# Kernel optimization log

Measured on AMD Instinct MI355X. Metric: run time of the kernel, lower is better.

The kernel has to match this reference:

```python
import jax, jax.numpy as jnp
import numpy as np

N_NODES = 3000
N_FEAT = 2
N_UNITS = 64
BATCH = 16
K_DIFF = 2  # max_diffusion_step


def _supports(adj):
    # dual_random_walk: (D^-1 A)^T and (D'^-1 A^T)^T, rows with zero degree -> 0
    def rw_T(A):
        d = A.sum(axis=1)
        d_inv = jnp.where(d > 0, 1.0 / d, 0.0)
        return (d_inv[:, None] * A).T  # (N, N)
    return [rw_T(adj), rw_T(adj.T)]


def _gconv(inputs, state, supports, W, b, num_nodes):
    # inputs: (B, N*F), state: (B, N*U)
    B = inputs.shape[0]
    x = jnp.concatenate([inputs.reshape(B, num_nodes, -1),
                         state.reshape(B, num_nodes, -1)], axis=2)  # (B, N, C)
    x0 = x.transpose(1, 2, 0)  # (N, C, B)
    mats = [x0]
    for S in supports:
        x1 = jnp.einsum('mn,ncb->mcb', S, x0)
        mats.append(x1)
        xk_1, xk_2 = x1, x0
        for _ in range(2, K_DIFF + 1):
            x2 = 2.0 * jnp.einsum('mn,ncb->mcb', S, xk_1) - xk_2  # Chebyshev recurrence
            mats.append(x2)
            xk_1, xk_2 = x2, xk_1
    xs = jnp.stack(mats, axis=0)  # (M, N, C, B)
    M, _, C, _ = xs.shape
    xs = xs.transpose(3, 1, 2, 0).reshape(B * num_nodes, C * M)
    out = xs @ W + b  # (B*N, O)
    return out.reshape(B, num_nodes * W.shape[1])


def setup_inputs() -> dict:
    key = jax.random.key(0)
    k1, k2, k3, k4, k5 = jax.random.split(key, 5)
    C = N_FEAT + N_UNITS          # 66
    M = 2 * K_DIFF + 1            # 5 (two supports)
    xw = lambda k, s: jax.random.normal(k, s, dtype=jnp.float32) * jnp.sqrt(2.0 / (s[0] + s[1]))
    return {
        "inputs": jax.random.normal(k1, (BATCH, N_NODES * N_FEAT), dtype=jnp.float32),
        "hx": jax.random.normal(k2, (BATCH, N_NODES * N_UNITS), dtype=jnp.float32),
        "adj_mx": jax.random.uniform(k3, (N_NODES, N_NODES), dtype=jnp.float32),
        "W_gate": xw(k4, (C * M, 2 * N_UNITS)),
        "b_gate": jnp.ones((2 * N_UNITS,), dtype=jnp.float32),  # bias_start=1.0
        "W_cand": xw(k5, (C * M, N_UNITS)),
        "b_cand": jnp.zeros((N_UNITS,), dtype=jnp.float32),
        "num_nodes": N_NODES,
    }


def reference(inputs, hx, adj_mx, W_gate, b_gate, W_cand, b_cand, num_nodes):
    supports = _supports(adj_mx)
    B = inputs.shape[0]
    value = jax.nn.sigmoid(_gconv(inputs, hx, supports, W_gate, b_gate, num_nodes))
    value = value.reshape(B, num_nodes, 2 * N_UNITS)
    r, u = value[..., :N_UNITS], value[..., N_UNITS:]
    r = r.reshape(B, num_nodes * N_UNITS)
    u = u.reshape(B, num_nodes * N_UNITS)
    c = jnp.tanh(_gconv(inputs, r * hx, supports, W_cand, b_cand, num_nodes))
    new_state = u * hx + (1.0 - u) * c
    return new_state
```

## Files before the change

kernel.cpp:

```cpp
#include <hip/hip_runtime.h>
#include <cstdint>
#include <cstddef>


typedef unsigned short u16;
typedef __bf16 bf16x8 __attribute__((ext_vector_type(8)));
typedef u16 u16x8 __attribute__((ext_vector_type(8)));
typedef u16 u16x4 __attribute__((ext_vector_type(4)));
typedef float f32x4 __attribute__((ext_vector_type(4)));

#define NND 3000
#define KP  3008
#define NBX 16
#define NCBP 1152
#define KW  330
#define KWP 352

__device__ __forceinline__ float b2f(u16 x) { return (float)__builtin_bit_cast(__bf16, x); }
__device__ __forceinline__ u16 f2b(float f) { return __builtin_bit_cast(u16, (__bf16)f); }

__device__ __forceinline__ int getmode(const u16* bgp) { return (bgp[0] == 0x3F80) ? 0 : 1; }

__device__ __forceinline__ float rdf(const void* p, size_t i, int mode) {
  return mode ? ((const float*)p)[i] : b2f(((const u16*)p)[i]);
}

__device__ __forceinline__ void gll16(const u16* g, void* l) {
  __builtin_amdgcn_global_load_lds(
      (const __attribute__((address_space(1))) unsigned int*)g,
      (__attribute__((address_space(3))) unsigned int*)l, 16, 0, 0);
}

__device__ __forceinline__ void ld4(const void* A, int rg, int cg, int mode,
                                    float& v0, float& v1, float& v2, float& v3) {
  v0 = v1 = v2 = v3 = 0.f;
  if (rg >= NND) return;
  if (cg + 3 < NND) {
    if (mode) {
      f32x4 f = *(const f32x4*)((const float*)A + (size_t)rg * NND + cg);
      v0 = f[0]; v1 = f[1]; v2 = f[2]; v3 = f[3];
    } else {
      u16x4 u = *(const u16x4*)((const u16*)A + (size_t)rg * NND + cg);
      v0 = b2f(u[0]); v1 = b2f(u[1]); v2 = b2f(u[2]); v3 = b2f(u[3]);
    }
  } else {
    if (cg + 0 < NND) v0 = rdf(A, (size_t)rg * NND + cg + 0, mode);
    if (cg + 1 < NND) v1 = rdf(A, (size_t)rg * NND + cg + 1, mode);
    if (cg + 2 < NND) v2 = rdf(A, (size_t)rg * NND + cg + 2, mode);
    if (cg + 3 < NND) v3 = rdf(A, (size_t)rg * NND + cg + 3, mode);
  }
}

struct PrepParams {
  const void* A;
  const void* Wg; const void* Wc;
  const void* inp; const void* hx;
  const u16* bgp;
  float* d0sum; float* d1sum;
  u16* Wtg; u16* Wtc;
  u16* xtg; u16* xtc; u16* chx;
};

__global__ __launch_bounds__(256) void k_prep(PrepParams p) {
  const int bid = blockIdx.x, t = threadIdx.x;
  const int mode = getmode(p.bgp);

  if (bid < 2209) {
    __shared__ float ldsx[64 * 65];
    const int R = (bid / 47) * 64, C = (bid % 47) * 64;
#pragma unroll
    for (int ph = 0; ph < 4; ++ph) {
      int idx = t + ph * 256;
      int r = idx >> 4, c4 = (idx & 15) * 4;
      float v0, v1, v2, v3;
      ld4(p.A, R + r, C + c4, mode, v0, v1, v2, v3);
      ldsx[r * 65 + c4 + 0] = v0;
      ldsx[r * 65 + c4 + 1] = v1;
      ldsx[r * 65 + c4 + 2] = v2;
      ldsx[r * 65 + c4 + 3] = v3;
    }
    __syncthreads();
    if (t < 64) {
      int rg = R + t;
      if (rg < NND) {
        float s = 0.f;
#pragma unroll 8
        for (int c = 0; c < 64; ++c) s += ldsx[t * 65 + c];
        atomicAdd(&p.d0sum[rg], s);
      }
    } else if (t < 128) {
      int cg = C + (t - 64);
      if (cg < NND) {
        float s = 0.f;
#pragma unroll 8
        for (int r = 0; r < 64; ++r) s += ldsx[r * 65 + (t - 64)];
        atomicAdd(&p.d1sum[cg], s);
      }
    }
    return;
  }
  if (bid < 2473) {
    const int idx = (bid - 2209) * 256 + t;
    if (idx < 128 * KWP) {
      int o = idx / KWP, k = idx - o * KWP;
      float v = (k < KW) ? rdf(p.Wg, (size_t)k * 128 + o, mode) : 0.f;
      p.Wtg[idx] = f2b(v);
    } else if (idx < 192 * KWP) {
      int i2 = idx - 128 * KWP;
      int o = i2 / KWP, k = i2 - o * KWP;
      float v = (k < KW) ? rdf(p.Wc, (size_t)k * 64 + o, mode) : 0.f;
      p.Wtc[i2] = f2b(v);
    }
    return;
  }
  {
    const int idx = bid - 2473;
    const int nt = idx % 24, b = idx / 24;
    const int n0 = nt * 128;
    __shared__ __align__(16) u16 hxl[128 * 72];
#pragma unroll
    for (int i = 0; i < 4; ++i) {
      int id = t + 256 * i;
      int nl = id >> 3, og = (id & 7) * 8;
      int ng = n0 + nl; if (ng > NND - 1) ng = NND - 1;
      const size_t base = (size_t)b * 192000 + (size_t)ng * 64 + og;
      u16x8 v;
      if (mode) {
        const float* h = (const float*)p.hx + base;
        f32x4 lo = *(const f32x4*)h, hi = *(const f32x4*)(h + 4);
        v[0] = f2b(lo[0]); v[1] = f2b(lo[1]); v[2] = f2b(lo[2]); v[3] = f2b(lo[3]);
        v[4] = f2b(hi[0]); v[5] = f2b(hi[1]); v[6] = f2b(hi[2]); v[7] = f2b(hi[3]);
      } else {
        v = *(const u16x8*)&((const u16*)p.hx)[base];
      }
      *(u16x8*)&hxl[nl * 72 + og] = v;
    }
    __syncthreads();
#pragma unroll
    for (int i = 0; i < 4; ++i) {
      int id = t + 256 * i;
      int nl = id >> 3, og = (id & 7) * 8;
      int ng = n0 + nl;
      if (ng < NND)
        *(u16x8*)&p.chx[(size_t)b * 192000 + (size_t)ng * 64 + og] = *(u16x8*)&hxl[nl * 72 + og];
    }
#pragma unroll
    for (int i = 0; i < 4; ++i) {
      int id = t + 256 * i;
      int u = id >> 4, ngrp = (id & 15) * 8;
      int nb = n0 + ngrp;
      if (nb < KP) {
        u16x8 v;
#pragma unroll
        for (int e = 0; e < 8; ++e) {
          int ng = nb + e;
          v[e] = (ng < NND) ? hxl[(ngrp + e) * 72 + u] : (u16)0;
        }
        *(u16x8*)&p.xtg[(size_t)((2 + u) * 16 + b) * KP + nb] = v;
      }
    }
    if (t < 32) {
      int c = t >> 4, ngrp = (t & 15) * 8;
      int nb = n0 + ngrp;
      if (nb < KP) {
        u16x8 v;
#pragma unroll
        for (int e = 0; e < 8; ++e) {
          int ng = nb + e;
          v[e] = (ng < NND) ? f2b(rdf(p.inp, (size_t)b * 6000 + (size_t)ng * 2 + c, mode)) : (u16)0;
        }
        *(u16x8*)&p.xtg[(size_t)(c * 16 + b) * KP + nb] = v;
        *(u16x8*)&p.xtc[(size_t)(c * 16 + b) * KP + nb] = v;
      }
    }
    if (nt == 23 && t < 64) {
      u16x8 z = {0, 0, 0, 0, 0, 0, 0, 0};
      *(u16x8*)&p.xtc[(size_t)((2 + t) * 16 + b) * KP + NND] = z;
    }
  }
}

__global__ __launch_bounds__(256) void k_sboth(const void* __restrict__ A, const float* __restrict__ d0sum,
                                               const float* __restrict__ d1sum,
                                               u16* __restrict__ S0, u16* __restrict__ S1,
                                               const u16* __restrict__ bgp) {
  __shared__ float ldsx[64 * 65];
  __shared__ float inv1c[64];
  __shared__ float inv0r[64];
  const int C = blockIdx.x * 64, R = blockIdx.y * 64, t = threadIdx.x;
  const int mode = getmode(bgp);
  if (t < 64) {
    int cg = C + t;
    float ds = (cg < NND) ? d1sum[cg] : 0.f;
    inv1c[t] = ds > 0.f ? 1.f / ds : 0.f;
  } else if (t < 128) {
    int rg = R + (t - 64);
    float ds = (rg < NND) ? d0sum[rg] : 0.f;
    inv0r[t - 64] = ds > 0.f ? 1.f / ds : 0.f;
  }
#pragma unroll
  for (int ph = 0; ph < 4; ++ph) {
    int idx = t + ph * 256;
    int r = idx >> 4, c4 = (idx & 15) * 4;
    float v0, v1, v2, v3;
    ld4(A, R + r, C + c4, mode, v0, v1, v2, v3);
    ldsx[r * 65 + c4 + 0] = v0;
    ldsx[r * 65 + c4 + 1] = v1;
    ldsx[r * 65 + c4 + 2] = v2;
    ldsx[r * 65 + c4 + 3] = v3;
  }
  __syncthreads();
#pragma unroll
  for (int ph = 0; ph < 4; ++ph) {
    int idx = t + ph * 256;
    int mr = idx >> 4, nc4 = (idx & 15) * 4;
    int m1 = R + mr;
    if (m1 < NND) {
      u16x4 v;
#pragma unroll
      for (int i = 0; i < 4; ++i) v[i] = f2b(ldsx[mr * 65 + nc4 + i] * inv1c[nc4 + i]);
      *(u16x4*)&S1[(size_t)m1 * KP + C + nc4] = v;
    }
    int m0_ = C + mr;
    if (m0_ < NND) {
      u16x4 v;
#pragma unroll
      for (int i = 0; i < 4; ++i) v[i] = f2b(ldsx[(nc4 + i) * 65 + mr] * inv0r[nc4 + i]);
      *(u16x4*)&S0[(size_t)m0_ * KP + R + nc4] = v;
    }
  }
}

struct GemmAParams {
  const u16* A0; const u16* A1;
  const u16* B0; const u16* B1;
  u16* D0; u16* D1;
  const u16* X;
  int mode;
};

__global__ __launch_bounds__(256, 2) void k_gemmA(GemmAParams p) {
  __shared__ __align__(16) u16 lds[32768];
  const int bid = blockIdx.x;
  const int x8 = bid & 7, g = bid >> 3;
  const int slot = g / 9, n_idx = g - slot * 9;
  const int strip = x8 * 6 + slot;
  const int m_idx = strip >> 1, z = strip & 1;
  const u16* Sp = z ? p.A1 : p.A0;
  const u16* Bp = z ? p.B1 : p.B0;
  u16* Dp = z ? p.D1 : p.D0;
  const int n0 = n_idx * 128;
  const int m0 = m_idx * 128;
  const int t = threadIdx.x;
  const int lane = t & 63, w = t >> 6;
  const int wr = w >> 1, wc = w & 1;
  const int l15 = lane & 15, lq = lane >> 4;
  const int x7 = l15 & 7;

  const u16* gsrc[8];
  int lbase[8];
#pragma unroll
  for (int q = 0; q < 8; ++q) {
    const int c = t + 256 * q;
    if (c < 1024) {
      const int row = c >> 3, grp = c & 7;
      int mg = m0 + row; if (mg > NND - 1) mg = NND - 1;
      gsrc[q] = Sp + (size_t)mg * KP + ((grp ^ (row & 7)) << 3);
      lbase[q] = q * 4096 + w * 1024;
    } else {
      const int c2 = c - 1024;
      const int row = c2 >> 3, grp = c2 & 7;
      gsrc[q] = Bp + (size_t)(n0 + row) * KP + ((grp ^ (row & 7)) << 3);
      lbase[q] = 16384 + (q - 4) * 4096 + w * 1024;
    }
  }

  f32x4 acc[4][4];
#pragma unroll
  for (int i = 0; i < 4; ++i)
#pragma unroll
    for (int j = 0; j < 4; ++j) acc[i][j] = (f32x4){0.f, 0.f, 0.f, 0.f};

  auto STAGE = [&](int buf) {
    char* L = (char*)lds + buf * 32768;
#pragma unroll
    for (int q = 0; q < 8; ++q) { gll16(gsrc[q], (void*)(L + lbase[q])); gsrc[q] += 64; }
  };
  auto STEP = [&](int buf) {
    const u16* L = lds + buf * 16384;
    bf16x8 af[4][2], bf[4][2];
#pragma unroll
    for (int kk = 0; kk < 2; ++kk) {
#pragma unroll
      for (int i = 0; i < 4; ++i)
        af[i][kk] = *(const bf16x8*)&L[(wr * 64 + i * 16 + l15) * 64 + (((kk * 4 + lq) ^ x7) << 3)];
#pragma unroll
      for (int j = 0; j < 4; ++j)
        bf[j][kk] = *(const bf16x8*)&L[8192 + (wc * 64 + j * 16 + l15) * 64 + (((kk * 4 + lq) ^ x7) << 3)];
    }
#pragma unroll
    for (int kk = 0; kk < 2; ++kk)
#pragma unroll
      for (int i = 0; i < 4; ++i)
#pragma unroll
        for (int j = 0; j < 4; ++j)
          acc[i][j] = __builtin_amdgcn_mfma_f32_16x16x32_bf16(af[i][kk], bf[j][kk], acc[i][j], 0, 0, 0);
  };

  STAGE(0);
  for (int ks = 0; ks < 47; ++ks) {
    const int buf = ks & 1;
    if (ks < 46) {
      STAGE(buf ^ 1);
      asm volatile("s_waitcnt vmcnt(8)" ::: "memory");
    } else {
      asm volatile("s_waitcnt vmcnt(0)" ::: "memory");
    }
    __builtin_amdgcn_s_barrier();
    __builtin_amdgcn_sched_barrier(0);
    STEP(buf);
    __builtin_amdgcn_sched_barrier(0);
    __builtin_amdgcn_s_barrier();
  }

  __syncthreads();
  u16* Tw = &lds[w * 4608];
#pragma unroll
  for (int i = 0; i < 4; ++i)
#pragma unroll
    for (int j = 0; j < 4; ++j)
#pragma unroll
      for (int r = 0; r < 4; ++r) {
        int miw = i * 16 + lq * 4 + r;
        int niw = j * 16 + l15;
        float v = acc[i][j][r];
        if (m0 + wr * 64 + miw >= NND) v = 0.f;
        Tw[niw * 72 + miw] = f2b(v);
      }
  const int row8 = lane >> 3, colg = (lane & 7) * 8;
#pragma unroll
  for (int ph = 0; ph < 8; ++ph) {
    int nrow = ph * 8 + row8;
    int n_g = n0 + wc * 64 + nrow;
    int m_b = m0 + wr * 64 + colg;
    if (m_b < KP) {
      u16x8 y = *(u16x8*)&Tw[nrow * 72 + colg];
      if (p.mode) {
        const u16x8 x = *(const u16x8*)&p.X[(size_t)n_g * KP + m_b];
#pragma unroll
        for (int e = 0; e < 8; ++e) y[e] = f2b(2.f * b2f(y[e]) - b2f(x[e]));
      }
      *(u16x8*)&Dp[(size_t)n_g * KP + m_b] = y;
    }
  }
}

struct GateParams {
  const u16* xall;
  const u16* Wt;
  const void* bias;
  const u16* hx;
  u16* xtc;
  u16* ut;
  const u16* bgp;
};

__global__ __launch_bounds__(256, 2) void k_gate(GateParams p) {
  __shared__ __align__(16) u16 Al[128 * 40];
  __shared__ __align__(16) u16 Bl[64 * 40];
  __shared__ __align__(16) u16 hxl[64 * 72];
  __shared__ int rowA[KWP];
  const int b = blockIdx.y, n0 = blockIdx.x * 64;
  const int t = threadIdx.x, lane = t & 63, w = t >> 6, wr = w >> 1, wc = w & 1;
  const int l15 = lane & 15, lq = lane >> 4;
  const int mode = getmode(p.bgp);

  for (int k = t; k < KWP; k += 256) {
    int c = k / 5, mt = k - c * 5;
    rowA[k] = (k < KW) ? (mt * NCBP + c * 16 + b) * KP : 0;
  }
#pragma unroll
  for (int i = 0; i < 2; ++i) {
    int id = t + 256 * i;
    int nl = id >> 3, og = (id & 7) * 8;
    int ng = n0 + nl; if (ng > NND - 1) ng = NND - 1;
    *(u16x8*)&hxl[nl * 72 + og] = *(const u16x8*)&p.hx[(size_t)b * 192000 + (size_t)ng * 64 + og];
  }
  __syncthreads();

  f32x4 acc[4][2];
#pragma unroll
  for (int i = 0; i < 4; ++i)
#pragma unroll
    for (int j = 0; j < 2; ++j) acc[i][j] = (f32x4){0.f, 0.f, 0.f, 0.f};

  u16x8 aReg[2]; u16x8 bReg;
#pragma unroll
  for (int hh = 0; hh < 2; ++hh) {
    int id = t + 256 * hh;
    int r = id >> 2, g = id & 3;
    aReg[hh] = *(const u16x8*)&p.Wt[(size_t)r * KWP + g * 8];
  }
#pragma unroll
  for (int e = 0; e < 8; ++e) {
    int k = w * 8 + e;
    u16 x = p.xall[(size_t)rowA[k] + n0 + lane];
    bReg[e] = (k < KW) ? x : (u16)0;
  }

  for (int ks = 0; ks < 11; ++ks) {
    __syncthreads();
#pragma unroll
    for (int hh = 0; hh < 2; ++hh) {
      int id = t + 256 * hh;
      int r = id >> 2, g = id & 3;
      *(u16x8*)&Al[r * 40 + g * 8] = aReg[hh];
    }
    *(u16x8*)&Bl[lane * 40 + w * 8] = bReg;
    __syncthreads();

    if (ks + 1 < 11) {
      const int k0 = (ks + 1) * 32;
#pragma unroll
      for (int hh = 0; hh < 2; ++hh) {
        int id = t + 256 * hh;
        int r = id >> 2, g = id & 3;
        aReg[hh] = *(const u16x8*)&p.Wt[(size_t)r * KWP + k0 + g * 8];
      }
#pragma unroll
      for (int e = 0; e < 8; ++e) {
        int k = k0 + w * 8 + e;
        u16 x = p.xall[(size_t)rowA[k] + n0 + lane];
        bReg[e] = (k < KW) ? x : (u16)0;
      }
    }

    bf16x8 af[4], bf[2];
#pragma unroll
    for (int i = 0; i < 4; ++i) af[i] = *(const bf16x8*)&Al[(wr * 64 + i * 16 + l15) * 40 + lq * 8];
#pragma unroll
    for (int j = 0; j < 2; ++j) bf[j] = *(const bf16x8*)&Bl[(wc * 32 + j * 16 + l15) * 40 + lq * 8];
#pragma unroll
    for (int i = 0; i < 4; ++i)
#pragma unroll
      for (int j = 0; j < 2; ++j)
        acc[i][j] = __builtin_amdgcn_mfma_f32_16x16x32_bf16(af[i], bf[j], acc[i][j], 0, 0, 0);
  }

#pragma unroll
  for (int i = 0; i < 4; ++i)
#pragma unroll
    for (int j = 0; j < 2; ++j)
#pragma unroll
      for (int r = 0; r < 4; ++r) {
        int o = wr * 64 + i * 16 + lq * 4 + r;
        int nl = wc * 32 + j * 16 + l15;
        int ng = n0 + nl;
        if (ng < NND) {
          float v = acc[i][j][r] + rdf(p.bias, o, mode);
          float s = 1.f / (1.f + __expf(-v));
          if (o < 64) {
            float rh = s * b2f(hxl[nl * 72 + o]);
            p.xtc[(size_t)((o + 2) * 16 + b) * KP + ng] = f2b(rh);
          } else {
            p.ut[(size_t)b * 192000 + (size_t)(o - 64) * NND + ng] = f2b(s);
          }
        }
      }
}

struct CandParams {
  const u16* xall;
  const u16* Wt;
  const void* bias;
  const u16* hx;
  const u16* ut;
  void* out;
  const u16* bgp;
};

__global__ __launch_bounds__(256, 2) void k_cand(CandParams p) {
  __shared__ __align__(16) u16 Al[64 * 40];
  __shared__ __align__(16) u16 Bl[64 * 40];
  __shared__ __align__(16) u16 hxl[64 * 72];
  __shared__ __align__(16) u16 newl[64 * 72];
  __shared__ int rowA[KWP];
  const int b = blockIdx.y, n0 = blockIdx.x * 64;
  const int t = threadIdx.x, lane = t & 63, w = t >> 6, wr = w >> 1, wc = w & 1;
  const int l15 = lane & 15, lq = lane >> 4;
  const int mode = getmode(p.bgp);

  for (int k = t; k < KWP; k += 256) {
    int c = k / 5, mt = k - c * 5;
    rowA[k] = (k < KW) ? (mt * NCBP + c * 16 + b) * KP : 0;
  }
#pragma unroll
  for (int i = 0; i < 2; ++i) {
    int id = t + 256 * i;
    int nl = id >> 3, og = (id & 7) * 8;
    int ng = n0 + nl; if (ng > NND - 1) ng = NND - 1;
    *(u16x8*)&hxl[nl * 72 + og] = *(const u16x8*)&p.hx[(size_t)b * 192000 + (size_t)ng * 64 + og];
  }
  __syncthreads();

  f32x4 acc[2][2];
#pragma unroll
  for (int i = 0; i < 2; ++i)
#pragma unroll
    for (int j = 0; j < 2; ++j) acc[i][j] = (f32x4){0.f, 0.f, 0.f, 0.f};

  u16x8 aReg; u16x8 bReg;
  {
    int r = t >> 2, g = t & 3;
    aReg = *(const u16x8*)&p.Wt[(size_t)r * KWP + g * 8];
  }
#pragma unroll
  for (int e = 0; e < 8; ++e) {
    int k = w * 8 + e;
    u16 x = p.xall[(size_t)rowA[k] + n0 + lane];
    bReg[e] = (k < KW) ? x : (u16)0;
  }

  for (int ks = 0; ks < 11; ++ks) {
    __syncthreads();
    {
      int r = t >> 2, g = t & 3;
      *(u16x8*)&Al[r * 40 + g * 8] = aReg;
    }
    *(u16x8*)&Bl[lane * 40 + w * 8] = bReg;
    __syncthreads();

    if (ks + 1 < 11) {
      const int k0 = (ks + 1) * 32;
      {
        int r = t >> 2, g = t & 3;
        aReg = *(const u16x8*)&p.Wt[(size_t)r * KWP + k0 + g * 8];
      }
#pragma unroll
      for (int e = 0; e < 8; ++e) {
        int k = k0 + w * 8 + e;
        u16 x = p.xall[(size_t)rowA[k] + n0 + lane];
        bReg[e] = (k < KW) ? x : (u16)0;
      }
    }

    bf16x8 af[2], bf[2];
#pragma unroll
    for (int i = 0; i < 2; ++i) af[i] = *(const bf16x8*)&Al[(wr * 32 + i * 16 + l15) * 40 + lq * 8];
#pragma unroll
    for (int j = 0; j < 2; ++j) bf[j] = *(const bf16x8*)&Bl[(wc * 32 + j * 16 + l15) * 40 + lq * 8];
#pragma unroll
    for (int i = 0; i < 2; ++i)
#pragma unroll
      for (int j = 0; j < 2; ++j)
        acc[i][j] = __builtin_amdgcn_mfma_f32_16x16x32_bf16(af[i], bf[j], acc[i][j], 0, 0, 0);
  }

#pragma unroll
  for (int i = 0; i < 2; ++i)
#pragma unroll
    for (int j = 0; j < 2; ++j)
#pragma unroll
      for (int r = 0; r < 4; ++r) {
        int o = wr * 32 + i * 16 + lq * 4 + r;
        int nl = wc * 32 + j * 16 + l15;
        int ng = n0 + nl; int ngc = ng > NND - 1 ? NND - 1 : ng;
        float v = acc[i][j][r] + rdf(p.bias, o, mode);
        float c = tanhf(v);
        float u = b2f(p.ut[(size_t)b * 192000 + (size_t)o * NND + ngc]);
        float h = b2f(hxl[nl * 72 + o]);
        newl[nl * 72 + o] = f2b(u * h + (1.f - u) * c);
      }
  __syncthreads();
#pragma unroll
  for (int i = 0; i < 2; ++i) {
    int id = t + 256 * i;
    int nl = id >> 3, og = (id & 7) * 8;
    int ng = n0 + nl;
    if (ng < NND) {
      u16x8 v = *(u16x8*)&newl[nl * 72 + og];
      if (mode) {
        float* of = (float*)p.out + (size_t)b * 192000 + (size_t)ng * 64 + og;
        f32x4 lo = {b2f(v[0]), b2f(v[1]), b2f(v[2]), b2f(v[3])};
        f32x4 hi = {b2f(v[4]), b2f(v[5]), b2f(v[6]), b2f(v[7])};
        *(f32x4*)of = lo;
        *(f32x4*)(of + 4) = hi;
      } else {
        *(u16x8*)&((u16*)p.out)[(size_t)b * 192000 + (size_t)ng * 64 + og] = v;
      }
    }
  }
}


extern "C" void kernel_launch(void* const* d_in, const int* in_sizes, int n_in,
                              void* d_out, int out_size, void* d_ws, size_t ws_size,
                              hipStream_t stream) {
  const size_t SLP = (size_t)NCBP * KP;
  size_t off = 0;
  auto alloc = [&](size_t bytes) {
    void* pp = (char*)d_ws + off;
    off += (bytes + 255) & ~(size_t)255;
    return pp;
  };
  u16* S0  = (u16*)alloc((size_t)NND * KP * 2);
  u16* S1  = (u16*)alloc((size_t)NND * KP * 2);
  u16* Xg  = (u16*)alloc(5 * SLP * 2);
  u16* Xc  = (u16*)alloc(5 * SLP * 2);
  u16* Ut  = (u16*)alloc((size_t)NBX * 64 * NND * 2);
  u16* Wtg = (u16*)alloc((size_t)128 * KWP * 2);
  u16* Wtc = (u16*)alloc((size_t)64 * KWP * 2);
  float* dsums = (float*)alloc(2 * NND * 4);
  u16* cHx  = (u16*)alloc((size_t)3072000 * 2);
  (void)in_sizes; (void)n_in; (void)out_size;

  if (ws_size < off) return;

  float* d0sum = dsums;
  float* d1sum = dsums + NND;

  u16* Xtg = Xg;            u16* Y1 = Xg + SLP;  u16* Z2 = Xg + 2 * SLP;
  u16* Y3 = Xg + 3 * SLP;   u16* Z4 = Xg + 4 * SLP;
  u16* Xtc = Xc;            u16* Y1c = Xc + SLP; u16* Z2c = Xc + 2 * SLP;
  u16* Y3c = Xc + 3 * SLP;  u16* Z4c = Xc + 4 * SLP;

  const void* inp = d_in[0];
  const void* hx  = d_in[1];
  const void* adj = d_in[2];
  const void* Wg  = d_in[3];
  const u16*  bg  = (const u16*)d_in[4];
  const void* Wc  = d_in[5];
  const void* bc  = d_in[6];

  hipMemsetAsync(dsums, 0, 2 * NND * 4, stream);
  PrepParams pp = {adj, Wg, Wc, inp, hx, bg, d0sum, d1sum, Wtg, Wtc, Xtg, Xtc, cHx};
  k_prep<<<2857, 256, 0, stream>>>(pp);
  k_sboth<<<dim3(47, 47), 256, 0, stream>>>(adj, d0sum, d1sum, S0, S1, bg);

  GemmAParams g1 = {S0, S1, Xtg, Xtg, Y1, Y3, nullptr, 0};
  k_gemmA<<<432, 256, 0, stream>>>(g1);
  GemmAParams g2 = {S0, S1, Y1, Y3, Z2, Z4, Xtg, 1};
  k_gemmA<<<432, 256, 0, stream>>>(g2);

  GateParams gp = {Xg, Wtg, bg, cHx, Xtc, Ut, bg};
  k_gate<<<dim3(47, NBX), 256, 0, stream>>>(gp);

  GemmAParams g3 = {S0, S1, Xtc, Xtc, Y1c, Y3c, nullptr, 0};
  k_gemmA<<<432, 256, 0, stream>>>(g3);
  GemmAParams g4 = {S0, S1, Y1c, Y3c, Z2c, Z4c, Xtc, 1};
  k_gemmA<<<432, 256, 0, stream>>>(g4);

  CandParams cp = {Xc, Wtc, bc, cHx, Ut, d_out, bg};
  k_cand<<<dim3(47, NBX), 256, 0, stream>>>(cp);
}
```

Baseline: 350.6 us.

## Fuse pipeline into one cooperative persistent kernel with grid syncs

Replaces the memset plus seven separate kernel launches with a single cooperative persistent kernel of 432 blocks. Stages are separated by grid.sync and each block loops over that stage's jobs. The degree sums are now computed directly instead of with atomics: a row reduction per warp and a strided column reduction. This removes launch gaps and the memset, but it caps parallelism at 432 blocks for the prep and S-build stages, and the column-sum walks memory in a strided pattern.

```diff
diff --git a/kernel.cpp b/kernel.cpp
--- a/kernel.cpp
+++ b/kernel.cpp
@@ -1,6 +1,9 @@
 #include <hip/hip_runtime.h>
+#include <hip/hip_cooperative_groups.h>
 #include <cstdint>
 #include <cstddef>
+
+namespace cg = cooperative_groups;
 
 
 typedef unsigned short u16;
@@ -15,6 +18,7 @@
 #define NCBP 1152
 #define KW  330
 #define KWP 352
+#define NBLK 432
 
 __device__ __forceinline__ float b2f(u16 x) { return (float)__builtin_bit_cast(__bf16, x); }
 __device__ __forceinline__ u16 f2b(float f) { return __builtin_bit_cast(u16, (__bf16)f); }
@@ -51,151 +55,156 @@
   }
 }
 
-struct PrepParams {
+struct MegaParams {
   const void* A;
   const void* Wg; const void* Wc;
   const void* inp; const void* hx;
   const u16* bgp;
+  const void* bcb;
   float* d0sum; float* d1sum;
   u16* Wtg; u16* Wtc;
-  u16* xtg; u16* xtc; u16* chx;
+  u16* Xg; u16* Xc;
+  u16* chx; u16* Ut;
+  u16* S0; u16* S1;
+  void* out;
 };
 
-__global__ __launch_bounds__(256) void k_prep(PrepParams p) {
-  const int bid = blockIdx.x, t = threadIdx.x;
-  const int mode = getmode(p.bgp);
-
-  if (bid < 2209) {
-    __shared__ float ldsx[64 * 65];
-    const int R = (bid / 47) * 64, C = (bid % 47) * 64;
-#pragma unroll
-    for (int ph = 0; ph < 4; ++ph) {
-      int idx = t + ph * 256;
-      int r = idx >> 4, c4 = (idx & 15) * 4;
-      float v0, v1, v2, v3;
-      ld4(p.A, R + r, C + c4, mode, v0, v1, v2, v3);
-      ldsx[r * 65 + c4 + 0] = v0;
-      ldsx[r * 65 + c4 + 1] = v1;
-      ldsx[r * 65 + c4 + 2] = v2;
-      ldsx[r * 65 + c4 + 3] = v3;
-    }
-    __syncthreads();
-    if (t < 64) {
-      int rg = R + t;
-      if (rg < NND) {
-        float s = 0.f;
-#pragma unroll 8
-        for (int c = 0; c < 64; ++c) s += ldsx[t * 65 + c];
-        atomicAdd(&p.d0sum[rg], s);
-      }
-    } else if (t < 128) {
-      int cg = C + (t - 64);
-      if (cg < NND) {
-        float s = 0.f;
-#pragma unroll 8
-        for (int r = 0; r < 64; ++r) s += ldsx[r * 65 + (t - 64)];
-        atomicAdd(&p.d1sum[cg], s);
-      }
-    }
-    return;
-  }
-  if (bid < 2473) {
-    const int idx = (bid - 2209) * 256 + t;
-    if (idx < 128 * KWP) {
-      int o = idx / KWP, k = idx - o * KWP;
-      float v = (k < KW) ? rdf(p.Wg, (size_t)k * 128 + o, mode) : 0.f;
-      p.Wtg[idx] = f2b(v);
-    } else if (idx < 192 * KWP) {
-      int i2 = idx - 128 * KWP;
-      int o = i2 / KWP, k = i2 - o * KWP;
-      float v = (k < KW) ? rdf(p.Wc, (size_t)k * 64 + o, mode) : 0.f;
-      p.Wtc[i2] = f2b(v);
-    }
-    return;
-  }
-  {
-    const int idx = bid - 2473;
-    const int nt = idx % 24, b = idx / 24;
-    const int n0 = nt * 128;
-    __shared__ __align__(16) u16 hxl[128 * 72];
-#pragma unroll
-    for (int i = 0; i < 4; ++i) {
-      int id = t + 256 * i;
-      int nl = id >> 3, og = (id & 7) * 8;
-      int ng = n0 + nl; if (ng > NND - 1) ng = NND - 1;
-      const size_t base = (size_t)b * 192000 + (size_t)ng * 64 + og;
+__device__ void prep_rowsum(int job, int t, int mode, const MegaParams& p) {
+  const int row = job * 4 + (t >> 6);
+  const int lane = t & 63;
+  float s = 0.f;
+  if (mode) {
+    const float* a = (const float*)p.A + (size_t)row * NND;
+    for (int i = lane; i < 750; i += 64) {
+      f32x4 v = *(const f32x4*)(a + 4 * i);
+      s += v[0] + v[1] + v[2] + v[3];
+    }
+  } else {
+    const u16* a = (const u16*)p.A + (size_t)row * NND;
+    for (int i = lane; i < 750; i += 64) {
+      u16x4 v = *(const u16x4*)(a + 4 * i);
+      s += b2f(v[0]) + b2f(v[1]) + b2f(v[2]) + b2f(v[3]);
+    }
+  }
+  for (int off = 32; off; off >>= 1) s += __shfl_down(s, off, 64);
+  if (lane == 0) p.d0sum[row] = s;
+}
+
+__device__ void prep_colsum(int job, int t, int mode, const MegaParams& p, u16* smem) {
+  float* red = (float*)smem;
+  const int c0 = job * 64;
+  const int lane = t & 63, g = t >> 6;
+  const int col = c0 + lane;
+  float s = 0.f;
+  if (col < NND) {
+    if (mode) {
+      const float* a = (const float*)p.A;
+      for (int rg = g; rg < NND; rg += 4) s += a[(size_t)rg * NND + col];
+    } else {
+      const u16* a = (const u16*)p.A;
+      for (int rg = g; rg < NND; rg += 4) s += b2f(a[(size_t)rg * NND + col]);
+    }
+  }
+  __syncthreads();
+  red[t] = s;
+  __syncthreads();
+  if (t < 64 && c0 + t < NND)
+    p.d1sum[c0 + t] = red[t] + red[t + 64] + red[t + 128] + red[t + 192];
+}
+
+__device__ void prep_wt2(int job, int t, int mode, const MegaParams& p) {
+  const int idx = job * 256 + t;
+  if (idx < 128 * KWP) {
+    int o = idx / KWP, k = idx - o * KWP;
+    float v = (k < KW) ? rdf(p.Wg, (size_t)k * 128 + o, mode) : 0.f;
+    p.Wtg[idx] = f2b(v);
+  } else if (idx < 192 * KWP) {
+    int i2 = idx - 128 * KWP;
+    int o = i2 / KWP, k = i2 - o * KWP;
+    float v = (k < KW) ? rdf(p.Wc, (size_t)k * 64 + o, mode) : 0.f;
+    p.Wtc[i2] = f2b(v);
+  }
+}
+
+__device__ void prep_buildx(int job, int t, int mode, const MegaParams& p, u16* smem) {
+  u16* hxl = smem;
+  const int nt = job % 24, b = job / 24;
+  const int n0 = nt * 128;
+  __syncthreads();
+#pragma unroll
+  for (int i = 0; i < 4; ++i) {
+    int id = t + 256 * i;
+    int nl = id >> 3, og = (id & 7) * 8;
+    int ng = n0 + nl; if (ng > NND - 1) ng = NND - 1;
+    const size_t base = (size_t)b * 192000 + (size_t)ng * 64 + og;
+    u16x8 v;
+    if (mode) {
+      const float* h = (const float*)p.hx + base;
+      f32x4 lo = *(const f32x4*)h, hi = *(const f32x4*)(h + 4);
+      v[0] = f2b(lo[0]); v[1] = f2b(lo[1]); v[2] = f2b(lo[2]); v[3] = f2b(lo[3]);
+      v[4] = f2b(hi[0]); v[5] = f2b(hi[1]); v[6] = f2b(hi[2]); v[7] = f2b(hi[3]);
+    } else {
+      v = *(const u16x8*)&((const u16*)p.hx)[base];
+    }
+    *(u16x8*)&hxl[nl * 72 + og] = v;
+  }
+  __syncthreads();
+#pragma unroll
+  for (int i = 0; i < 4; ++i) {
+    int id = t + 256 * i;
+    int nl = id >> 3, og = (id & 7) * 8;
+    int ng = n0 + nl;
+    if (ng < NND)
+      *(u16x8*)&p.chx[(size_t)b * 192000 + (size_t)ng * 64 + og] = *(u16x8*)&hxl[nl * 72 + og];
+  }
+#pragma unroll
+  for (int i = 0; i < 4; ++i) {
+    int id = t + 256 * i;
+    int u = id >> 4, ngrp = (id & 15) * 8;
+    int nb = n0 + ngrp;
+    if (nb < KP) {
       u16x8 v;
-      if (mode) {
-        const float* h = (const float*)p.hx + base;
-        f32x4 lo = *(const f32x4*)h, hi = *(const f32x4*)(h + 4);
-        v[0] = f2b(lo[0]); v[1] = f2b(lo[1]); v[2] = f2b(lo[2]); v[3] = f2b(lo[3]);
-        v[4] = f2b(hi[0]); v[5] = f2b(hi[1]); v[6] = f2b(hi[2]); v[7] = f2b(hi[3]);
-      } else {
-        v = *(const u16x8*)&((const u16*)p.hx)[base];
-      }
-      *(u16x8*)&hxl[nl * 72 + og] = v;
-    }
-    __syncthreads();
-#pragma unroll
-    for (int i = 0; i < 4; ++i) {
-      int id = t + 256 * i;
-      int nl = id >> 3, og = (id & 7) * 8;
-      int ng = n0 + nl;
-      if (ng < NND)
-        *(u16x8*)&p.chx[(size_t)b * 192000 + (size_t)ng * 64 + og] = *(u16x8*)&hxl[nl * 72 + og];
-    }
-#pragma unroll
-    for (int i = 0; i < 4; ++i) {
-      int id = t + 256 * i;
-      int u = id >> 4, ngrp = (id & 15) * 8;
-      int nb = n0 + ngrp;
-      if (nb < KP) {
-        u16x8 v;
-#pragma unroll
-        for (int e = 0; e < 8; ++e) {
-          int ng = nb + e;
-          v[e] = (ng < NND) ? hxl[(ngrp + e) * 72 + u] : (u16)0;
-        }
-        *(u16x8*)&p.xtg[(size_t)((2 + u) * 16 + b) * KP + nb] = v;
-      }
-    }
-    if (t < 32) {
-      int c = t >> 4, ngrp = (t & 15) * 8;
-      int nb = n0 + ngrp;
-      if (nb < KP) {
-        u16x8 v;
-#pragma unroll
-        for (int e = 0; e < 8; ++e) {
-          int ng = nb + e;
-          v[e] = (ng < NND) ? f2b(rdf(p.inp, (size_t)b * 6000 + (size_t)ng * 2 + c, mode)) : (u16)0;
-        }
-        *(u16x8*)&p.xtg[(size_t)(c * 16 + b) * KP + nb] = v;
-        *(u16x8*)&p.xtc[(size_t)(c * 16 + b) * KP + nb] = v;
-      }
-    }
-    if (nt == 23 && t < 64) {
-      u16x8 z = {0, 0, 0, 0, 0, 0, 0, 0};
-      *(u16x8*)&p.xtc[(size_t)((2 + t) * 16 + b) * KP + NND] = z;
-    }
-  }
-}
-
-__global__ __launch_bounds__(256) void k_sboth(const void* __restrict__ A, const float* __restrict__ d0sum,
-                                               const float* __restrict__ d1sum,
-                                               u16* __restrict__ S0, u16* __restrict__ S1,
-                                               const u16* __restrict__ bgp) {
-  __shared__ float ldsx[64 * 65];
-  __shared__ float inv1c[64];
-  __shared__ float inv0r[64];
-  const int C = blockIdx.x * 64, R = blockIdx.y * 64, t = threadIdx.x;
-  const int mode = getmode(bgp);
+#pragma unroll
+      for (int e = 0; e < 8; ++e) {
+        int ng = nb + e;
+        v[e] = (ng < NND) ? hxl[(ngrp + e) * 72 + u] : (u16)0;
+      }
+      *(u16x8*)&p.Xg[(size_t)((2 + u) * 16 + b) * KP + nb] = v;
+    }
+  }
+  if (t < 32) {
+    int c = t >> 4, ngrp = (t & 15) * 8;
+    int nb = n0 + ngrp;
+    if (nb < KP) {
+      u16x8 v;
+#pragma unroll
+      for (int e = 0; e < 8; ++e) {
+        int ng = nb + e;
+        v[e] = (ng < NND) ? f2b(rdf(p.inp, (size_t)b * 6000 + (size_t)ng * 2 + c, mode)) : (u16)0;
+      }
+      *(u16x8*)&p.Xg[(size_t)(c * 16 + b) * KP + nb] = v;
+      *(u16x8*)&p.Xc[(size_t)(c * 16 + b) * KP + nb] = v;
+    }
+  }
+  if (nt == 23 && t < 64) {
+    u16x8 z = {0, 0, 0, 0, 0, 0, 0, 0};
+    *(u16x8*)&p.Xc[(size_t)((2 + t) * 16 + b) * KP + NND] = z;
+  }
+}
+
+__device__ void sboth_job(int job, int t, int mode, const MegaParams& p, u16* smem) {
+  float* ldsx = (float*)smem;
+  float* inv1c = ldsx + 64 * 65;
+  float* inv0r = inv1c + 64;
+  const int C = (job % 47) * 64, R = (job / 47) * 64;
+  __syncthreads();
   if (t < 64) {
     int cg = C + t;
-    float ds = (cg < NND) ? d1sum[cg] : 0.f;
+    float ds = (cg < NND) ? p.d1sum[cg] : 0.f;
     inv1c[t] = ds > 0.f ? 1.f / ds : 0.f;
   } else if (t < 128) {
     int rg = R + (t - 64);
-    float ds = (rg < NND) ? d0sum[rg] : 0.f;
+    float ds = (rg < NND) ? p.d0sum[rg] : 0.f;
     inv0r[t - 64] = ds > 0.f ? 1.f / ds : 0.f;
   }
 #pragma unroll
@@ -203,7 +212,7 @@
     int idx = t + ph * 256;
     int r = idx >> 4, c4 = (idx & 15) * 4;
     float v0, v1, v2, v3;
-    ld4(A, R + r, C + c4, mode, v0, v1, v2, v3);
+    ld4(p.A, R + r, C + c4, mode, v0, v1, v2, v3);
     ldsx[r * 65 + c4 + 0] = v0;
     ldsx[r * 65 + c4 + 1] = v1;
     ldsx[r * 65 + c4 + 2] = v2;
@@ -219,39 +228,31 @@
       u16x4 v;
 #pragma unroll
       for (int i = 0; i < 4; ++i) v[i] = f2b(ldsx[mr * 65 + nc4 + i] * inv1c[nc4 + i]);
-      *(u16x4*)&S1[(size_t)m1 * KP + C + nc4] = v;
+      *(u16x4*)&p.S1[(size_t)m1 * KP + C + nc4] = v;
     }
     int m0_ = C + mr;
     if (m0_ < NND) {
       u16x4 v;
 #pragma unroll
       for (int i = 0; i < 4; ++i) v[i] = f2b(ldsx[(nc4 + i) * 65 + mr] * inv0r[nc4 + i]);
-      *(u16x4*)&S0[(size_t)m0_ * KP + R + nc4] = v;
-    }
-  }
-}
-
-struct GemmAParams {
-  const u16* A0; const u16* A1;
-  const u16* B0; const u16* B1;
-  u16* D0; u16* D1;
-  const u16* X;
-  int mode;
-};
-
-__global__ __launch_bounds__(256, 2) void k_gemmA(GemmAParams p) {
-  __shared__ __align__(16) u16 lds[32768];
-  const int bid = blockIdx.x;
+      *(u16x4*)&p.S0[(size_t)m0_ * KP + R + nc4] = v;
+    }
+  }
+}
+
+__device__ void gemm_job(int bid, int t,
+                         const u16* A0, const u16* A1,
+                         const u16* B0, const u16* B1,
+                         u16* D0, u16* D1, const u16* X, int xmode, u16* ldsp) {
   const int x8 = bid & 7, g = bid >> 3;
   const int slot = g / 9, n_idx = g - slot * 9;
   const int strip = x8 * 6 + slot;
   const int m_idx = strip >> 1, z = strip & 1;
-  const u16* Sp = z ? p.A1 : p.A0;
-  const u16* Bp = z ? p.B1 : p.B0;
-  u16* Dp = z ? p.D1 : p.D0;
+  const u16* Sp = z ? A1 : A0;
+  const u16* Bp = z ? B1 : B0;
+  u16* Dp = z ? D1 : D0;
   const int n0 = n_idx * 128;
   const int m0 = m_idx * 128;
-  const int t = threadIdx.x;
   const int lane = t & 63, w = t >> 6;
   const int wr = w >> 1, wc = w & 1;
   const int l15 = lane & 15, lq = lane >> 4;
@@ -282,12 +283,12 @@
     for (int j = 0; j < 4; ++j) acc[i][j] = (f32x4){0.f, 0.f, 0.f, 0.f};
 
   auto STAGE = [&](int buf) {
-    char* L = (char*)lds + buf * 32768;
+    char* L = (char*)ldsp + buf * 32768;
 #pragma unroll
     for (int q = 0; q < 8; ++q) { gll16(gsrc[q], (void*)(L + lbase[q])); gsrc[q] += 64; }
   };
   auto STEP = [&](int buf) {
-    const u16* L = lds + buf * 16384;
+    const u16* L = ldsp + buf * 16384;
     bf16x8 af[4][2], bf[4][2];
 #pragma unroll
     for (int kk = 0; kk < 2; ++kk) {
@@ -324,7 +325,7 @@
   }
 
   __syncthreads();
-  u16* Tw = &lds[w * 4608];
+  u16* Tw = &ldsp[w * 4608];
 #pragma unroll
   for (int i = 0; i < 4; ++i)
 #pragma unroll
@@ -345,8 +346,8 @@
     int m_b = m0 + wr * 64 + colg;
     if (m_b < KP) {
       u16x8 y = *(u16x8*)&Tw[nrow * 72 + colg];
-      if (p.mode) {
-        const u16x8 x = *(const u16x8*)&p.X[(size_t)n_g * KP + m_b];
+      if (xmode) {
+        const u16x8 x = *(const u16x8*)&X[(size_t)n_g * KP + m_b];
 #pragma unroll
         for (int e = 0; e < 8; ++e) y[e] = f2b(2.f * b2f(y[e]) - b2f(x[e]));
       }
@@ -355,25 +356,15 @@
   }
 }
 
-struct GateParams {
-  const u16* xall;
-  const u16* Wt;
-  const void* bias;
-  const u16* hx;
-  u16* xtc;
-  u16* ut;
-  const u16* bgp;
-};
-
-__global__ __launch_bounds__(256, 2) void k_gate(GateParams p) {
-  __shared__ __align__(16) u16 Al[128 * 40];
-  __shared__ __align__(16) u16 Bl[64 * 40];
-  __shared__ __align__(16) u16 hxl[64 * 72];
-  __shared__ int rowA[KWP];
-  const int b = blockIdx.y, n0 = blockIdx.x * 64;
-  const int t = threadIdx.x, lane = t & 63, w = t >> 6, wr = w >> 1, wc = w & 1;
+__device__ void gate_job(int job, int t, int mode, const MegaParams& p, u16* smem) {
+  u16* Al = smem;
+  u16* Bl = smem + 128 * 40;
+  u16* hxl = Bl + 64 * 40;
+  int* rowA = (int*)(hxl + 64 * 72);
+  const int b = job / 47, n0 = (job % 47) * 64;
+  const int lane = t & 63, w = t >> 6, wr = w >> 1, wc = w & 1;
   const int l15 = lane & 15, lq = lane >> 4;
-  const int mode = getmode(p.bgp);
+  __syncthreads();
 
   for (int k = t; k < KWP; k += 256) {
     int c = k / 5, mt = k - c * 5;
@@ -384,7 +375,7 @@
     int id = t + 256 * i;
     int nl = id >> 3, og = (id & 7) * 8;
     int ng = n0 + nl; if (ng > NND - 1) ng = NND - 1;
-    *(u16x8*)&hxl[nl * 72 + og] = *(const u16x8*)&p.hx[(size_t)b * 192000 + (size_t)ng * 64 + og];
+    *(u16x8*)&hxl[nl * 72 + og] = *(const u16x8*)&p.chx[(size_t)b * 192000 + (size_t)ng * 64 + og];
   }
   __syncthreads();
 
@@ -399,12 +390,12 @@
   for (int hh = 0; hh < 2; ++hh) {
     int id = t + 256 * hh;
     int r = id >> 2, g = id & 3;
-    aReg[hh] = *(const u16x8*)&p.Wt[(size_t)r * KWP + g * 8];
+    aReg[hh] = *(const u16x8*)&p.Wtg[(size_t)r * KWP + g * 8];
   }
 #pragma unroll
   for (int e = 0; e < 8; ++e) {
     int k = w * 8 + e;
-    u16 x = p.xall[(size_t)rowA[k] + n0 + lane];
+    u16 x = p.Xg[(size_t)rowA[k] + n0 + lane];
     bReg[e] = (k < KW) ? x : (u16)0;
   }
 
@@ -425,12 +416,12 @@
       for (int hh = 0; hh < 2; ++hh) {
         int id = t + 256 * hh;
         int r = id >> 2, g = id & 3;
-        aReg[hh] = *(const u16x8*)&p.Wt[(size_t)r * KWP + k0 + g * 8];
+        aReg[hh] = *(const u16x8*)&p.Wtg[(size_t)r * KWP + k0 + g * 8];
       }
 #pragma unroll
       for (int e = 0; e < 8; ++e) {
         int k = k0 + w * 8 + e;
-        u16 x = p.xall[(size_t)rowA[k] + n0 + lane];
+        u16 x = p.Xg[(size_t)rowA[k] + n0 + lane];
         bReg[e] = (k < KW) ? x : (u16)0;
       }
     }
@@ -457,38 +448,28 @@
         int nl = wc * 32 + j * 16 + l15;
         int ng = n0 + nl;
         if (ng < NND) {
-          float v = acc[i][j][r] + rdf(p.bias, o, mode);
+          float v = acc[i][j][r] + rdf(p.bgp, o, mode);
           float s = 1.f / (1.f + __expf(-v));
           if (o < 64) {
             float rh = s * b2f(hxl[nl * 72 + o]);
-            p.xtc[(size_t)((o + 2) * 16 + b) * KP + ng] = f2b(rh);
+            p.Xc[(size_t)((o + 2) * 16 + b) * KP + ng] = f2b(rh);
           } else {
-            p.ut[(size_t)b * 192000 + (size_t)(o - 64) * NND + ng] = f2b(s);
+            p.Ut[(size_t)b * 192000 + (size_t)(o - 64) * NND + ng] = f2b(s);
           }
         }
       }
 }
 
-struct CandParams {
-  const u16* xall;
-  const u16* Wt;
-  const void* bias;
-  const u16* hx;
-  const u16* ut;
-  void* out;
-  const u16* bgp;
-};
-
-__global__ __launch_bounds__(256, 2) void k_cand(CandParams p) {
-  __shared__ __align__(16) u16 Al[64 * 40];
-  __shared__ __align__(16) u16 Bl[64 * 40];
-  __shared__ __align__(16) u16 hxl[64 * 72];
-  __shared__ __align__(16) u16 newl[64 * 72];
-  __shared__ int rowA[KWP];
-  const int b = blockIdx.y, n0 = blockIdx.x * 64;
-  const int t = threadIdx.x, lane = t & 63, w = t >> 6, wr = w >> 1, wc = w & 1;
+__device__ void cand_job(int job, int t, int mode, const MegaParams& p, u16* smem) {
+  u16* Al = smem;
+  u16* Bl = smem + 64 * 40;
+  u16* hxl = Bl + 64 * 40;
+  u16* newl = hxl + 64 * 72;
+  int* rowA = (int*)(newl + 64 * 72);
+  const int b = job / 47, n0 = (job % 47) * 64;
+  const int lane = t & 63, w = t >> 6, wr = w >> 1, wc = w & 1;
   const int l15 = lane & 15, lq = lane >> 4;
-  const int mode = getmode(p.bgp);
+  __syncthreads();
 
   for (int k = t; k < KWP; k += 256) {
     int c = k / 5, mt = k - c * 5;
@@ -499,7 +480,7 @@
     int id = t + 256 * i;
     int nl = id >> 3, og = (id & 7) * 8;
     int ng = n0 + nl; if (ng > NND - 1) ng = NND - 1;
-    *(u16x8*)&hxl[nl * 72 + og] = *(const u16x8*)&p.hx[(size_t)b * 192000 + (size_t)ng * 64 + og];
+    *(u16x8*)&hxl[nl * 72 + og] = *(const u16x8*)&p.chx[(size_t)b * 192000 + (size_t)ng * 64 + og];
   }
   __syncthreads();
 
@@ -512,12 +493,12 @@
   u16x8 aReg; u16x8 bReg;
   {
     int r = t >> 2, g = t & 3;
-    aReg = *(const u16x8*)&p.Wt[(size_t)r * KWP + g * 8];
+    aReg = *(const u16x8*)&p.Wtc[(size_t)r * KWP + g * 8];
   }
 #pragma unroll
   for (int e = 0; e < 8; ++e) {
     int k = w * 8 + e;
-    u16 x = p.xall[(size_t)rowA[k] + n0 + lane];
+    u16 x = p.Xc[(size_t)rowA[k] + n0 + lane];
     bReg[e] = (k < KW) ? x : (u16)0;
   }
 
@@ -534,12 +515,12 @@
       const int k0 = (ks + 1) * 32;
       {
         int r = t >> 2, g = t & 3;
-        aReg = *(const u16x8*)&p.Wt[(size_t)r * KWP + k0 + g * 8];
+        aReg = *(const u16x8*)&p.Wtc[(size_t)r * KWP + k0 + g * 8];
       }
 #pragma unroll
       for (int e = 0; e < 8; ++e) {
         int k = k0 + w * 8 + e;
-        u16 x = p.xall[(size_t)rowA[k] + n0 + lane];
+        u16 x = p.Xc[(size_t)rowA[k] + n0 + lane];
         bReg[e] = (k < KW) ? x : (u16)0;
       }
     }
@@ -565,9 +546,9 @@
         int o = wr * 32 + i * 16 + lq * 4 + r;
         int nl = wc * 32 + j * 16 + l15;
         int ng = n0 + nl; int ngc = ng > NND - 1 ? NND - 1 : ng;
-        float v = acc[i][j][r] + rdf(p.bias, o, mode);
+        float v = acc[i][j][r] + rdf(p.bcb, o, mode);
         float c = tanhf(v);
-        float u = b2f(p.ut[(size_t)b * 192000 + (size_t)o * NND + ngc]);
+        float u = b2f(p.Ut[(size_t)b * 192000 + (size_t)o * NND + ngc]);
         float h = b2f(hxl[nl * 72 + o]);
         newl[nl * 72 + o] = f2b(u * h + (1.f - u) * c);
       }
@@ -590,6 +571,86 @@
       }
     }
   }
+}
+
+__device__ __forceinline__ void slabs(const MegaParams& p,
+                                      u16*& Xtg, u16*& Y1, u16*& Z2, u16*& Y3, u16*& Z4,
+                                      u16*& Xtc, u16*& Y1c, u16*& Z2c, u16*& Y3c, u16*& Z4c) {
+  const size_t SLP = (size_t)NCBP * KP;
+  Xtg = p.Xg;            Y1 = p.Xg + SLP;  Z2 = p.Xg + 2 * SLP;
+  Y3 = p.Xg + 3 * SLP;   Z4 = p.Xg + 4 * SLP;
+  Xtc = p.Xc;            Y1c = p.Xc + SLP; Z2c = p.Xc + 2 * SLP;
+  Y3c = p.Xc + 3 * SLP;  Z4c = p.Xc + 4 * SLP;
+}
+
+__global__ __launch_bounds__(256, 2) void k_mega(MegaParams p) {
+  __shared__ __align__(16) u16 smem[32768];
+  cg::grid_group grid = cg::this_grid();
+  const int bid = blockIdx.x, t = threadIdx.x;
+  const int mode = getmode(p.bgp);
+  u16 *Xtg, *Y1, *Z2, *Y3, *Z4, *Xtc, *Y1c, *Z2c, *Y3c, *Z4c;
+  slabs(p, Xtg, Y1, Z2, Y3, Z4, Xtc, Y1c, Z2c, Y3c, Z4c);
+
+  for (int job = bid; job < 1445; job += NBLK) {
+    if (job < 750)       prep_rowsum(job, t, mode, p);
+    else if (job < 797)  prep_colsum(job - 750, t, mode, p, smem);
+    else if (job < 1061) prep_wt2(job - 797, t, mode, p);
+    else                 prep_buildx(job - 1061, t, mode, p, smem);
+  }
+  grid.sync();
+
+  for (int job = bid; job < 2209; job += NBLK) sboth_job(job, t, mode, p, smem);
+  grid.sync();
+
+  gemm_job(bid, t, p.S0, p.S1, Xtg, Xtg, Y1, Y3, nullptr, 0, smem);
+  grid.sync();
+  gemm_job(bid, t, p.S0, p.S1, Y1, Y3, Z2, Z4, Xtg, 1, smem);
+  grid.sync();
+
+  for (int job = bid; job < 752; job += NBLK) gate_job(job, t, mode, p, smem);
+  grid.sync();
+
+  gemm_job(bid, t, p.S0, p.S1, Xtc, Xtc, Y1c, Y3c, nullptr, 0, smem);
+  grid.sync();
+  gemm_job(bid, t, p.S0, p.S1, Y1c, Y3c, Z2c, Z4c, Xtc, 1, smem);
+  grid.sync();
+
+  for (int job = bid; job < 752; job += NBLK) cand_job(job, t, mode, p, smem);
+}
+
+__global__ __launch_bounds__(256) void fb_prep(MegaParams p) {
+  __shared__ __align__(16) u16 smem[9216];
+  const int job = blockIdx.x, t = threadIdx.x;
+  const int mode = getmode(p.bgp);
+  if (job < 750)       prep_rowsum(job, t, mode, p);
+  else if (job < 797)  prep_colsum(job - 750, t, mode, p, smem);
+  else if (job < 1061) prep_wt2(job - 797, t, mode, p);
+  else                 prep_buildx(job - 1061, t, mode, p, smem);
+}
+
+__global__ __launch_bounds__(256) void fb_sboth(MegaParams p) {
+  __shared__ __align__(16) u16 smem[8576];
+  sboth_job(blockIdx.x, threadIdx.x, getmode(p.bgp), p, smem);
+}
+
+__global__ __launch_bounds__(256, 2) void fb_gemm(MegaParams p, int which) {
+  __shared__ __align__(16) u16 smem[32768];
+  u16 *Xtg, *Y1, *Z2, *Y3, *Z4, *Xtc, *Y1c, *Z2c, *Y3c, *Z4c;
+  slabs(p, Xtg, Y1, Z2, Y3, Z4, Xtc, Y1c, Z2c, Y3c, Z4c);
+  if (which == 0)      gemm_job(blockIdx.x, threadIdx.x, p.S0, p.S1, Xtg, Xtg, Y1, Y3, nullptr, 0, smem);
+  else if (which == 1) gemm_job(blockIdx.x, threadIdx.x, p.S0, p.S1, Y1, Y3, Z2, Z4, Xtg, 1, smem);
+  else if (which == 2) gemm_job(blockIdx.x, threadIdx.x, p.S0, p.S1, Xtc, Xtc, Y1c, Y3c, nullptr, 0, smem);
+  else                 gemm_job(blockIdx.x, threadIdx.x, p.S0, p.S1, Y1c, Y3c, Z2c, Z4c, Xtc, 1, smem);
+}
+
+__global__ __launch_bounds__(256, 2) void fb_gate(MegaParams p) {
+  __shared__ __align__(16) u16 smem[12992];
+  gate_job(blockIdx.x, threadIdx.x, getmode(p.bgp), p, smem);
+}
+
+__global__ __launch_bounds__(256, 2) void fb_cand(MegaParams p) {
+  __shared__ __align__(16) u16 smem[15040];
+  cand_job(blockIdx.x, threadIdx.x, getmode(p.bgp), p, smem);
 }
 
 
@@ -616,40 +677,44 @@
 
   if (ws_size < off) return;
 
-  float* d0sum = dsums;
-  float* d1sum = dsums + NND;
-
-  u16* Xtg = Xg;            u16* Y1 = Xg + SLP;  u16* Z2 = Xg + 2 * SLP;
-  u16* Y3 = Xg + 3 * SLP;   u16* Z4 = Xg + 4 * SLP;
-  u16* Xtc = Xc;            u16* Y1c = Xc + SLP; u16* Z2c = Xc + 2 * SLP;
-  u16* Y3c = Xc + 3 * SLP;  u16* Z4c = Xc + 4 * SLP;
-
-  const void* inp = d_in[0];
-  const void* hx  = d_in[1];
-  const void* adj = d_in[2];
-  const void* Wg  = d_in[3];
-  const u16*  bg  = (const u16*)d_in[4];
-  const void* Wc  = d_in[5];
-  const void* bc  = d_in[6];
-
-  hipMemsetAsync(dsums, 0, 2 * NND * 4, stream);
-  PrepParams pp = {adj, Wg, Wc, inp, hx, bg, d0sum, d1sum, Wtg, Wtc, Xtg, Xtc, cHx};
-  k_prep<<<2857, 256, 0, stream>>>(pp);
-  k_sboth<<<dim3(47, 47), 256, 0, stream>>>(adj, d0sum, d1sum, S0, S1, bg);
-
-  GemmAParams g1 = {S0, S1, Xtg, Xtg, Y1, Y3, nullptr, 0};
-  k_gemmA<<<432, 256, 0, stream>>>(g1);
-  GemmAParams g2 = {S0, S1, Y1, Y3, Z2, Z4, Xtg, 1};
-  k_gemmA<<<432, 256, 0, stream>>>(g2);
-
-  GateParams gp = {Xg, Wtg, bg, cHx, Xtc, Ut, bg};
-  k_gate<<<dim3(47, NBX), 256, 0, stream>>>(gp);
-
-  GemmAParams g3 = {S0, S1, Xtc, Xtc, Y1c, Y3c, nullptr, 0};
-  k_gemmA<<<432, 256, 0, stream>>>(g3);
-  GemmAParams g4 = {S0, S1, Y1c, Y3c, Z2c, Z4c, Xtc, 1};
-  k_gemmA<<<432, 256, 0, stream>>>(g4);
-
-  CandParams cp = {Xc, Wtc, bc, cHx, Ut, d_out, bg};
-  k_cand<<<dim3(47, NBX), 256, 0, stream>>>(cp);
-}
+  MegaParams mp;
+  mp.A = d_in[2]; mp.Wg = d_in[3]; mp.Wc = d_in[5];
+  mp.inp = d_in[0]; mp.hx = d_in[1];
+  mp.bgp = (const u16*)d_in[4]; mp.bcb = d_in[6];
+  mp.d0sum = dsums; mp.d1sum = dsums + NND;
+  mp.Wtg = Wtg; mp.Wtc = Wtc;
+  mp.Xg = Xg; mp.Xc = Xc;
+  mp.chx = cHx; mp.Ut = Ut;
+  mp.S0 = S0; mp.S1 = S1;
+  mp.out = d_out;
+
+  static int s_coop = -1;
+  if (s_coop < 0) {
+    int dev = 0;
+    (void)hipGetDevice(&dev);
+    int attr = 0;
+    if (hipDeviceGetAttribute(&attr, hipDeviceAttributeCooperativeLaunch, dev) != hipSuccess) attr = 0;
+    int maxb = 0;
+    if (attr) {
+      if (hipOccupancyMaxActiveBlocksPerMultiprocessor(&maxb, k_mega, 256, 0) != hipSuccess) maxb = 0;
+    }
+    s_coop = (attr && maxb >= 2) ? 1 : 0;
+  }
+
+  bool did_coop = false;
+  if (s_coop) {
+    void* args[] = { (void*)&mp };
+    hipError_t e = hipLaunchCooperativeKernel((void*)k_mega, dim3(NBLK), dim3(256), args, 0, stream);
+    did_coop = (e == hipSuccess);
+  }
+  if (!did_coop) {
+    fb_prep<<<1445, 256, 0, stream>>>(mp);
+    fb_sboth<<<2209, 256, 0, stream>>>(mp);
+    fb_gemm<<<NBLK, 256, 0, stream>>>(mp, 0);
+    fb_gemm<<<NBLK, 256, 0, stream>>>(mp, 1);
+    fb_gate<<<752, 256, 0, stream>>>(mp);
+    fb_gemm<<<NBLK, 256, 0, stream>>>(mp, 2);
+    fb_gemm<<<NBLK, 256, 0, stream>>>(mp, 3);
+    fb_cand<<<752, 256, 0, stream>>>(mp);
+  }
+}
```

Result: slower. 576.0 us (+64.3%).

## Replace atomic tiled degree sums with direct row/column reductions, drop memset

Applied to the files above, without the earlier changes.

Degree computation in the prep kernel no longer uses 2209 tiles that transpose through LDS and atomically add partial sums. Row sums now come from one wavefront per row with vector loads and a shuffle reduction. Column sums come from 47 blocks, each striding down all rows for 64 columns and reducing through shared memory. Since every sum is written exactly once, the memset and the atomics go away, but the column-sum phase runs on only 47 blocks, each with a long serial loop.

```diff
diff --git a/kernel.cpp b/kernel.cpp
--- a/kernel.cpp
+++ b/kernel.cpp
@@ -62,45 +62,55 @@
 };
 
 __global__ __launch_bounds__(256) void k_prep(PrepParams p) {
+  __shared__ __align__(16) u16 smem[9216];
   const int bid = blockIdx.x, t = threadIdx.x;
   const int mode = getmode(p.bgp);
 
-  if (bid < 2209) {
-    __shared__ float ldsx[64 * 65];
-    const int R = (bid / 47) * 64, C = (bid % 47) * 64;
-#pragma unroll
-    for (int ph = 0; ph < 4; ++ph) {
-      int idx = t + ph * 256;
-      int r = idx >> 4, c4 = (idx & 15) * 4;
-      float v0, v1, v2, v3;
-      ld4(p.A, R + r, C + c4, mode, v0, v1, v2, v3);
-      ldsx[r * 65 + c4 + 0] = v0;
-      ldsx[r * 65 + c4 + 1] = v1;
-      ldsx[r * 65 + c4 + 2] = v2;
-      ldsx[r * 65 + c4 + 3] = v3;
+  if (bid < 750) {
+    const int row = bid * 4 + (t >> 6);
+    const int lane = t & 63;
+    float s = 0.f;
+    if (mode) {
+      const float* a = (const float*)p.A + (size_t)row * NND;
+      for (int i = lane; i < 750; i += 64) {
+        f32x4 v = *(const f32x4*)(a + 4 * i);
+        s += v[0] + v[1] + v[2] + v[3];
+      }
+    } else {
+      const u16* a = (const u16*)p.A + (size_t)row * NND;
+      for (int i = lane; i < 750; i += 64) {
+        u16x4 v = *(const u16x4*)(a + 4 * i);
+        s += b2f(v[0]) + b2f(v[1]) + b2f(v[2]) + b2f(v[3]);
+      }
+    }
+    for (int off = 32; off; off >>= 1) s += __shfl_down(s, off, 64);
+    if (lane == 0) p.d0sum[row] = s;
+    return;
+  }
+  if (bid < 797) {
+    float* red = (float*)smem;
+    const int c0 = (bid - 750) * 64;
+    const int lane = t & 63, g = t >> 6;
+    const int col = c0 + lane;
+    float s = 0.f;
+    if (col < NND) {
+      if (mode) {
+        const float* a = (const float*)p.A;
+        for (int rg = g; rg < NND; rg += 4) s += a[(size_t)rg * NND + col];
+      } else {
+        const u16* a = (const u16*)p.A;
+        for (int rg = g; rg < NND; rg += 4) s += b2f(a[(size_t)rg * NND + col]);
+      }
     }
     __syncthreads();
-    if (t < 64) {
-      int rg = R + t;
-      if (rg < NND) {
-        float s = 0.f;
-#pragma unroll 8
-        for (int c = 0; c < 64; ++c) s += ldsx[t * 65 + c];
-        atomicAdd(&p.d0sum[rg], s);
-      }
-    } else if (t < 128) {
-      int cg = C + (t - 64);
-      if (cg < NND) {
-        float s = 0.f;
-#pragma unroll 8
-        for (int r = 0; r < 64; ++r) s += ldsx[r * 65 + (t - 64)];
-        atomicAdd(&p.d1sum[cg], s);
-      }
-    }
+    red[t] = s;
+    __syncthreads();
+    if (t < 64 && c0 + t < NND)
+      p.d1sum[c0 + t] = red[t] + red[t + 64] + red[t + 128] + red[t + 192];
     return;
   }
-  if (bid < 2473) {
-    const int idx = (bid - 2209) * 256 + t;
+  if (bid < 1061) {
+    const int idx = (bid - 797) * 256 + t;
     if (idx < 128 * KWP) {
       int o = idx / KWP, k = idx - o * KWP;
       float v = (k < KW) ? rdf(p.Wg, (size_t)k * 128 + o, mode) : 0.f;
@@ -114,10 +124,10 @@
     return;
   }
   {
-    const int idx = bid - 2473;
+    u16* hxl = smem;
+    const int idx = bid - 1061;
     const int nt = idx % 24, b = idx / 24;
     const int n0 = nt * 128;
-    __shared__ __align__(16) u16 hxl[128 * 72];
 #pragma unroll
     for (int i = 0; i < 4; ++i) {
       int id = t + 256 * i;
@@ -632,9 +642,8 @@
   const void* Wc  = d_in[5];
   const void* bc  = d_in[6];
 
-  hipMemsetAsync(dsums, 0, 2 * NND * 4, stream);
   PrepParams pp = {adj, Wg, Wc, inp, hx, bg, d0sum, d1sum, Wtg, Wtc, Xtg, Xtc, cHx};
-  k_prep<<<2857, 256, 0, stream>>>(pp);
+  k_prep<<<1445, 256, 0, stream>>>(pp);
   k_sboth<<<dim3(47, 47), 256, 0, stream>>>(adj, d0sum, d1sum, S0, S1, bg);
 
   GemmAParams g1 = {S0, S1, Xtg, Xtg, Y1, Y3, nullptr, 0};
```

Measured after the change: 538.3 us. 1.54x slower.
